# Optimization experiments

Hardware: AMD Instinct MI355X
Metric: run time of the kernel (lower is better)

The kernel has to match this reference:

```python
import jax, jax.numpy as jnp
import numpy as np

N_EMBD = 1024
N_HEADS = 16
HEAD_SIZE = N_EMBD // N_HEADS
BLOCK_SIZE = 2048
BATCH = 2
SEQ = 2048
EPS = 1e-5


def setup_inputs() -> dict:
    key = jax.random.key(0)
    ks = jax.random.split(key, 12)
    s = 0.02
    x = jax.random.normal(ks[0], (BATCH, SEQ, N_EMBD), dtype=jnp.float32)
    # per-head Q/K/V weights concatenated: [n_embd, n_heads*head_size]
    Wq = jax.random.normal(ks[1], (N_EMBD, N_EMBD), dtype=jnp.float32) * s
    Wk = jax.random.normal(ks[2], (N_EMBD, N_EMBD), dtype=jnp.float32) * s
    Wv = jax.random.normal(ks[3], (N_EMBD, N_EMBD), dtype=jnp.float32) * s
    Wproj = jax.random.normal(ks[4], (N_EMBD, N_EMBD), dtype=jnp.float32) * s
    bproj = jnp.zeros((N_EMBD,), dtype=jnp.float32)
    W1 = jax.random.normal(ks[5], (N_EMBD, 4 * N_EMBD), dtype=jnp.float32) * s
    b1 = jnp.zeros((4 * N_EMBD,), dtype=jnp.float32)
    W2 = jax.random.normal(ks[6], (4 * N_EMBD, N_EMBD), dtype=jnp.float32) * s
    b2 = jnp.zeros((N_EMBD,), dtype=jnp.float32)
    ln1_w = jnp.ones((N_EMBD,), dtype=jnp.float32)
    ln1_b = jnp.zeros((N_EMBD,), dtype=jnp.float32)
    ln2_w = jnp.ones((N_EMBD,), dtype=jnp.float32)
    ln2_b = jnp.zeros((N_EMBD,), dtype=jnp.float32)
    return dict(x=x, Wq=Wq, Wk=Wk, Wv=Wv, Wproj=Wproj, bproj=bproj,
                W1=W1, b1=b1, W2=W2, b2=b2,
                ln1_w=ln1_w, ln1_b=ln1_b, ln2_w=ln2_w, ln2_b=ln2_b)


def _layer_norm(x, w, b):
    mu = jnp.mean(x, axis=-1, keepdims=True)
    var = jnp.var(x, axis=-1, keepdims=True)
    return (x - mu) * jax.lax.rsqrt(var + EPS) * w + b


def reference(x, Wq, Wk, Wv, Wproj, bproj, W1, b1, W2, b2, ln1_w, ln1_b, ln2_w, ln2_b):
    B, T, C = x.shape
    # --- attention sub-block (pre-LN) ---
    h = _layer_norm(x, ln1_w, ln1_b)
    # project then split heads: [B,T,H,D] -> [B,H,T,D]
    def split(W):
        return (h @ W).reshape(B, T, N_HEADS, HEAD_SIZE).transpose(0, 2, 1, 3)
    q, k, v = split(Wq), split(Wk), split(Wv)
    # NOTE: original code scales by C**-0.5 with C = n_embd (not head_size)
    scores = jnp.einsum('bhtd,bhsd->bhts', q, k) * (C ** -0.5)  # [B,H,T,T]
    causal = jnp.tril(jnp.ones((T, T), dtype=bool))
    scores = jnp.where(causal, scores, -jnp.inf)
    wei = jax.nn.softmax(scores, axis=-1)
    attn = jnp.einsum('bhts,bhsd->bhtd', wei, v)  # [B,H,T,D]
    attn = attn.transpose(0, 2, 1, 3).reshape(B, T, C)  # concat heads
    x = x + attn @ Wproj + bproj
    # --- FFN sub-block (pre-LN) ---
    h2 = _layer_norm(x, ln2_w, ln2_b)
    ff = jax.nn.relu(h2 @ W1 + b1) @ W2 + b2
    return x + ff
```

## Files before the change

### kernel.cpp

```cpp
#include <hip/hip_runtime.h>
#include <cstdint>

typedef __attribute__((ext_vector_type(8))) __bf16 bf16_8;
typedef __attribute__((ext_vector_type(4))) __bf16 bf16_4;
typedef __attribute__((ext_vector_type(4))) float f32x4;

#define QSCALE 0.045084220027780106f

__device__ __forceinline__ void gld_lds16(const __bf16* g, __bf16* l) {
  __builtin_amdgcn_global_load_lds(
      (const __attribute__((address_space(1))) void*)(void*)g,
      (__attribute__((address_space(3))) void*)l, 16, 0, 0);
}

__global__ __launch_bounds__(256) void convt_k(
    const float* __restrict__ Wq, const float* __restrict__ Wk,
    const float* __restrict__ Wv, const float* __restrict__ Wp,
    const float* __restrict__ W1, const float* __restrict__ W2,
    __bf16* __restrict__ WqT, __bf16* __restrict__ WkT,
    __bf16* __restrict__ WvT, __bf16* __restrict__ WpT,
    __bf16* __restrict__ W1T, __bf16* __restrict__ W2T) {
  int bid = blockIdx.x;
  const float* in; __bf16* outp; int Kd, Nd, tile;
  if (bid < 4096) {
    int m = bid >> 10; tile = bid & 1023; Kd = 1024; Nd = 1024;
    in   = m == 0 ? Wq  : m == 1 ? Wk  : m == 2 ? Wv  : Wp;
    outp = m == 0 ? WqT : m == 1 ? WkT : m == 2 ? WvT : WpT;
  } else if (bid < 8192) {
    tile = bid - 4096; Kd = 1024; Nd = 4096; in = W1; outp = W1T;
  } else {
    tile = bid - 8192; Kd = 4096; Nd = 1024; in = W2; outp = W2T;
  }
  int tilesN = Nd >> 5;
  int tk = tile / tilesN, tn = tile % tilesN;
  int k0 = tk * 32, n0 = tn * 32;
  __shared__ float tbuf[32][33];
  int tx = threadIdx.x & 31, ty = threadIdx.x >> 5;
#pragma unroll
  for (int i = 0; i < 4; ++i)
    tbuf[ty + i * 8][tx] = in[(size_t)(k0 + ty + i * 8) * Nd + (n0 + tx)];
  __syncthreads();
#pragma unroll
  for (int i = 0; i < 4; ++i)
    outp[(size_t)(n0 + ty + i * 8) * Kd + (k0 + tx)] = (__bf16)tbuf[tx][ty + i * 8];
}

__global__ __launch_bounds__(256) void ln_k(const float* __restrict__ x,
                                            const float* __restrict__ w,
                                            const float* __restrict__ b,
                                            __bf16* __restrict__ out) {
  int row = blockIdx.x;
  int tid = threadIdx.x;
  f32x4 v = *(const f32x4*)(x + (size_t)row * 1024 + tid * 4);
  float s = v[0] + v[1] + v[2] + v[3];
  float sq = v[0] * v[0] + v[1] * v[1] + v[2] * v[2] + v[3] * v[3];
#pragma unroll
  for (int m = 1; m < 64; m <<= 1) { s += __shfl_xor(s, m); sq += __shfl_xor(sq, m); }
  __shared__ float rs[4], rq[4];
  int wave = tid >> 6, lane = tid & 63;
  if (lane == 0) { rs[wave] = s; rq[wave] = sq; }
  __syncthreads();
  s  = rs[0] + rs[1] + rs[2] + rs[3];
  sq = rq[0] + rq[1] + rq[2] + rq[3];
  float mu   = s * (1.f / 1024.f);
  float var  = sq * (1.f / 1024.f) - mu * mu;
  float rstd = rsqrtf(var + 1e-5f);
  f32x4 wv = *(const f32x4*)(w + tid * 4);
  f32x4 bv = *(const f32x4*)(b + tid * 4);
  bf16_4 o;
#pragma unroll
  for (int i = 0; i < 4; ++i) o[i] = (__bf16)((v[i] - mu) * rstd * wv[i] + bv[i]);
  *(bf16_4*)(out + (size_t)row * 1024 + tid * 4) = o;
}

template <int MODE, int BM, int BN, int BK>
__global__ __launch_bounds__(256) void gemm_k(
    const __bf16* __restrict__ A,
    const __bf16* __restrict__ B0, const __bf16* __restrict__ B1,
    const __bf16* __restrict__ B2,
    __bf16* __restrict__ O0, __bf16* __restrict__ O1, __bf16* __restrict__ O2,
    float* __restrict__ Of,
    const float* __restrict__ bias, const float* __restrict__ res,
    int K, int Nchunk, int nBlkM, int nBlkN) {
  constexpr int NC = BK / 8;
  constexpr int MT = BM / 32, NT = BN / 32;
  constexpr int KK = BK / 32;
  constexpr int RPC = 64 / NC;
  constexpr int CA = BM / RPC / 4;
  constexpr int CB = BN / RPC / 4;
  __shared__ __align__(16) __bf16 As[2][BM * BK];
  __shared__ __align__(16) __bf16 Bs[2][BN * BK];
  int chunk = blockIdx.y;
  const __bf16* Bt = chunk == 0 ? B0 : (chunk == 1 ? B1 : B2);
  __bf16* Ob       = chunk == 0 ? O0 : (chunk == 1 ? O1 : O2);
  int pid = blockIdx.x;
  const int GM = 8;
  int perG = GM * nBlkN;
  int gid = pid / perG;
  int fm = gid * GM;
  int gsz = min(nBlkM - fm, GM);
  int bm = fm + (pid % gsz);
  int bn = (pid % perG) / gsz;
  int m0 = bm * BM, n0 = bn * BN;
  int tid = threadIdx.x, wave = tid >> 6, lane = tid & 63;
  int quad = lane >> 4, l16 = lane & 15;
  int wm = (wave & 1) * (BM / 2), wn = (wave >> 1) * (BN / 2);
  int srow = lane / NC, schunk = lane % NC;

  f32x4 z = {0.f, 0.f, 0.f, 0.f};
  f32x4 acc[MT][NT];
#pragma unroll
  for (int mt = 0; mt < MT; ++mt)
#pragma unroll
    for (int nt = 0; nt < NT; ++nt) acc[mt][nt] = z;

  const __bf16* Ag = A  + (size_t)m0 * K;
  const __bf16* Bg = Bt + (size_t)n0 * K;

  auto stage = [&](int k0, int buf) {
#pragma unroll
    for (int i = 0; i < CA; ++i) {
      int r0 = (wave * CA + i) * RPC;
      int gc = schunk ^ ((r0 + srow) & (NC - 1));
      gld_lds16(Ag + (size_t)(r0 + srow) * K + k0 + gc * 8, &As[buf][r0 * BK]);
    }
#pragma unroll
    for (int i = 0; i < CB; ++i) {
      int r0 = (wave * CB + i) * RPC;
      int gc = schunk ^ ((r0 + srow) & (NC - 1));
      gld_lds16(Bg + (size_t)(r0 + srow) * K + k0 + gc * 8, &Bs[buf][r0 * BK]);
    }
  };

  auto compute = [&](int buf) {
#pragma unroll
    for (int kk = 0; kk < KK; ++kk) {
      bf16_8 af[MT], bfr[NT];
#pragma unroll
      for (int t = 0; t < MT; ++t) {
        int r = wm + t * 16 + l16;
        int lc = (kk * 4 + quad) ^ (r & (NC - 1));
        af[t] = *(const bf16_8*)(&As[buf][r * BK + lc * 8]);
      }
#pragma unroll
      for (int t = 0; t < NT; ++t) {
        int r = wn + t * 16 + l16;
        int lc = (kk * 4 + quad) ^ (r & (NC - 1));
        bfr[t] = *(const bf16_8*)(&Bs[buf][r * BK + lc * 8]);
      }
#pragma unroll
      for (int mt = 0; mt < MT; ++mt)
#pragma unroll
        for (int nt = 0; nt < NT; ++nt)
          acc[mt][nt] = __builtin_amdgcn_mfma_f32_16x16x32_bf16(af[mt], bfr[nt],
                                                                acc[mt][nt], 0, 0, 0);
    }
  };

  int niter = K / BK;
  stage(0, 0);
  __syncthreads();
  for (int it = 0; it < niter - 1; ++it) {
    stage((it + 1) * BK, (it + 1) & 1);
    compute(it & 1);
    __syncthreads();
  }
  compute((niter - 1) & 1);

  if (MODE == 0 && chunk == 2) {
#pragma unroll
    for (int mt = 0; mt < MT; ++mt) {
      int mbase = m0 + wm + mt * 16 + quad * 4;
      int bb = mbase >> 11, tt = mbase & 2047;
#pragma unroll
      for (int nt = 0; nt < NT; ++nt) {
        int n = n0 + wn + nt * 16 + l16;
        bf16_4 pk;
#pragma unroll
        for (int r = 0; r < 4; ++r) pk[r] = (__bf16)acc[mt][nt][r];
        *(bf16_4*)(O2 + ((size_t)((bb * 16 + (n >> 6)) * 64 + (n & 63))) * 2048 + tt) = pk;
      }
    }
    return;
  }

  float oscale = (MODE == 0 && chunk == 0) ? QSCALE : 1.0f;
#pragma unroll
  for (int mt = 0; mt < MT; ++mt) {
#pragma unroll
    for (int r = 0; r < 4; ++r) {
      int m = m0 + wm + mt * 16 + quad * 4 + r;
      size_t rowo = (size_t)m * Nchunk;
#pragma unroll
      for (int nt = 0; nt < NT; ++nt) {
        int n = n0 + wn + nt * 16 + l16;
        float v = acc[mt][nt][r];
        if (MODE == 0) {
          Ob[rowo + n] = (__bf16)(v * oscale);
        } else if (MODE == 1) {
          v += bias[n]; v = v > 0.f ? v : 0.f;
          Ob[rowo + n] = (__bf16)v;
        } else {
          v += bias[n] + res[rowo + n];
          Of[rowo + n] = v;
        }
      }
    }
  }
}

__global__ __launch_bounds__(256) void attn_k(const __bf16* __restrict__ Q,
                                              const __bf16* __restrict__ K,
                                              const __bf16* __restrict__ Vt,
                                              __bf16* __restrict__ O) {
  __shared__ __align__(16) __bf16 Pls[4][32 * 72];
  __shared__ __align__(16) float Obuf[2][32][68];
  __shared__ float Lbuf[2][32][4];

  int i = blockIdx.x;
  int bh = i & 31, p = i >> 5;
  int h = bh & 15, b = bh >> 4;
  int tid = threadIdx.x, wave = tid >> 6, lane = tid & 63;
  int quad = lane >> 4, l16 = lane & 15;
  int pr = wave >> 1;
  int roleB = wave & 1;
  int j = pr == 0 ? p : 31 - p;
  int qg_lo = j, qg_hi = 63 - j;
  int t_lo = (j >> 1) + 1;
  int t_hi = 32 - (j >> 1);
  int ksp = 17 - t_lo;

  const __bf16* Kb = K + (size_t)(b * 2048) * 1024 + h * 64;
  const __bf16* Vh = Vt + (size_t)((b * 16 + h) * 64) * 2048;
  __bf16* Pw = &Pls[wave][0];

  f32x4 z = {0.f, 0.f, 0.f, 0.f};
  bf16_8 qf[2][2];
  f32x4 ot[2][4];
  float l_acc[2];

  auto loadQ = [&](int qg) {
#pragma unroll
    for (int g = 0; g < 2; ++g) {
      const __bf16* Qg = Q + ((size_t)(b * 2048 + qg * 32 + g * 16 + l16)) * 1024 + h * 64;
      qf[g][0] = *(const bf16_8*)(Qg + quad * 8);
      qf[g][1] = *(const bf16_8*)(Qg + 32 + quad * 8);
    }
  };

  auto zacc = [&]() {
#pragma unroll
    for (int g = 0; g < 2; ++g) {
#pragma unroll
      for (int dt = 0; dt < 4; ++dt) ot[g][dt] = z;
      l_acc[g] = 0.f;
    }
  };

  auto process = [&](int qg, int it0, int it1) {
    int qw = qg * 32;
    for (int it = it0; it < it1; ++it) {
      int kt = it * 64;
      bool masked = (kt + 63 > qw);
      bf16_8 kfr[4][2], vfr[4][2];
#pragma unroll
      for (int kk = 0; kk < 4; ++kk) {
        const __bf16* kr = Kb + (size_t)(kt + kk * 16 + l16) * 1024 + quad * 8;
        kfr[kk][0] = *(const bf16_8*)(kr);
        kfr[kk][1] = *(const bf16_8*)(kr + 32);
      }
#pragma unroll
      for (int dt = 0; dt < 4; ++dt) {
        const __bf16* vr = Vh + (size_t)(dt * 16 + l16) * 2048 + kt + quad * 8;
        vfr[dt][0] = *(const bf16_8*)(vr);
        vfr[dt][1] = *(const bf16_8*)(vr + 32);
      }
      f32x4 sf[2][4];
#pragma unroll
      for (int kk = 0; kk < 4; ++kk) {
#pragma unroll
        for (int g = 0; g < 2; ++g) {
          f32x4 a = z;
          a = __builtin_amdgcn_mfma_f32_16x16x32_bf16(kfr[kk][0], qf[g][0], a, 0, 0, 0);
          a = __builtin_amdgcn_mfma_f32_16x16x32_bf16(kfr[kk][1], qf[g][1], a, 0, 0, 0);
          sf[g][kk] = a;
        }
      }
#pragma unroll
      for (int g = 0; g < 2; ++g) {
        int qrow = qw + g * 16 + l16;
#pragma unroll
        for (int kk = 0; kk < 4; ++kk) {
          bf16_4 pk;
#pragma unroll
          for (int r = 0; r < 4; ++r) {
            float x = sf[g][kk][r];
            if (masked && (kt + kk * 16 + quad * 4 + r > qrow)) x = -1e30f;
            float pp = __builtin_amdgcn_exp2f(x);
            l_acc[g] += pp;
            pk[r] = (__bf16)pp;
          }
          *(bf16_4*)(Pw + (g * 16 + l16) * 72 + kk * 16 + quad * 4) = pk;
        }
      }
      bf16_8 pf[2][2];
#pragma unroll
      for (int g = 0; g < 2; ++g) {
        pf[g][0] = *(const bf16_8*)(Pw + (g * 16 + l16) * 72 + quad * 8);
        pf[g][1] = *(const bf16_8*)(Pw + (g * 16 + l16) * 72 + 32 + quad * 8);
      }
#pragma unroll
      for (int dt = 0; dt < 4; ++dt) {
#pragma unroll
        for (int g = 0; g < 2; ++g) {
          ot[g][dt] = __builtin_amdgcn_mfma_f32_16x16x32_bf16(vfr[dt][0], pf[g][0], ot[g][dt], 0, 0, 0);
          ot[g][dt] = __builtin_amdgcn_mfma_f32_16x16x32_bf16(vfr[dt][1], pf[g][1], ot[g][dt], 0, 0, 0);
        }
      }
    }
  };

  auto writeO = [&](int qg, const float* lc) {
#pragma unroll
    for (int g = 0; g < 2; ++g) {
      float l = lc[g];
      l += __shfl_xor(l, 16);
      l += __shfl_xor(l, 32);
      float inv = 1.0f / l;
      size_t base = (size_t)(b * 2048 + qg * 32 + g * 16 + l16) * 1024 + h * 64;
#pragma unroll
      for (int dt = 0; dt < 4; ++dt) {
        bf16_4 ok;
#pragma unroll
        for (int r = 0; r < 4; ++r) ok[r] = (__bf16)(ot[g][dt][r] * inv);
        *(bf16_4*)(O + base + dt * 16 + quad * 4) = ok;
      }
    }
  };

  if (roleB) {
    loadQ(qg_hi); zacc();
    process(qg_hi, ksp, t_hi);
#pragma unroll
    for (int g = 0; g < 2; ++g) {
#pragma unroll
      for (int dt = 0; dt < 4; ++dt)
        *(f32x4*)&Obuf[pr][g * 16 + l16][dt * 16 + quad * 4] = ot[g][dt];
      Lbuf[pr][g * 16 + l16][quad] = l_acc[g];
    }
  } else {
    loadQ(qg_lo); zacc();
    process(qg_lo, 0, t_lo);
    writeO(qg_lo, l_acc);
    loadQ(qg_hi); zacc();
    process(qg_hi, 0, ksp);
  }
  __syncthreads();
  if (!roleB) {
#pragma unroll
    for (int g = 0; g < 2; ++g) {
#pragma unroll
      for (int dt = 0; dt < 4; ++dt)
        ot[g][dt] += *(const f32x4*)&Obuf[pr][g * 16 + l16][dt * 16 + quad * 4];
    }
    float lc[2];
#pragma unroll
    for (int g = 0; g < 2; ++g) lc[g] = l_acc[g] + Lbuf[pr][g * 16 + l16][quad];
    writeO(qg_hi, lc);
  }
}

extern "C" void kernel_launch(void* const* d_in, const int* in_sizes, int n_in,
                              void* d_out, int out_size, void* d_ws,
                              size_t ws_size, hipStream_t stream) {
  const float* x   = (const float*)d_in[0];
  const float* Wq  = (const float*)d_in[1];
  const float* Wk  = (const float*)d_in[2];
  const float* Wv  = (const float*)d_in[3];
  const float* Wp  = (const float*)d_in[4];
  const float* bp  = (const float*)d_in[5];
  const float* W1  = (const float*)d_in[6];
  const float* b1  = (const float*)d_in[7];
  const float* W2  = (const float*)d_in[8];
  const float* b2  = (const float*)d_in[9];
  const float* l1w = (const float*)d_in[10];
  const float* l1b = (const float*)d_in[11];
  const float* l2w = (const float*)d_in[12];
  const float* l2b = (const float*)d_in[13];
  float* out = (float*)d_out;
  char* ws = (char*)d_ws;
  const size_t MB = 1024ull * 1024ull;
  __bf16* WqT = (__bf16*)(ws + 0 * MB);
  __bf16* WkT = (__bf16*)(ws + 2 * MB);
  __bf16* WvT = (__bf16*)(ws + 4 * MB);
  __bf16* WpT = (__bf16*)(ws + 6 * MB);
  __bf16* W1T = (__bf16*)(ws + 8 * MB);
  __bf16* W2T = (__bf16*)(ws + 16 * MB);
  __bf16* hb  = (__bf16*)(ws + 24 * MB);
  __bf16* Qb  = (__bf16*)(ws + 32 * MB);
  __bf16* Kb_ = (__bf16*)(ws + 40 * MB);
  __bf16* Vt  = (__bf16*)(ws + 48 * MB);
  __bf16* Ab  = (__bf16*)(ws + 56 * MB);
  __bf16* F1  = (__bf16*)(ws + 64 * MB);

  convt_k<<<12288, 256, 0, stream>>>(Wq, Wk, Wv, Wp, W1, W2,
                                     WqT, WkT, WvT, WpT, W1T, W2T);
  ln_k<<<4096, 256, 0, stream>>>(x, l1w, l1b, hb);
  gemm_k<0, 128, 128, 32><<<dim3(256, 3), 256, 0, stream>>>(
      hb, WqT, WkT, WvT, Qb, Kb_, Vt, nullptr, nullptr, nullptr,
      1024, 1024, 32, 8);
  attn_k<<<512, 256, 0, stream>>>(Qb, Kb_, Vt, Ab);
  gemm_k<2, 64, 64, 64><<<dim3(1024, 1), 256, 0, stream>>>(
      Ab, WpT, WpT, WpT, nullptr, nullptr, nullptr, out, bp, x,
      1024, 1024, 64, 16);
  ln_k<<<4096, 256, 0, stream>>>(out, l2w, l2b, hb);
  gemm_k<1, 128, 128, 32><<<dim3(1024, 1), 256, 0, stream>>>(
      hb, W1T, W1T, W1T, F1, F1, F1, nullptr, b1, nullptr,
      1024, 4096, 32, 32);
  gemm_k<2, 64, 64, 64><<<dim3(1024, 1), 256, 0, stream>>>(
      F1, W2T, W2T, W2T, nullptr, nullptr, nullptr, out, b2, out,
      4096, 1024, 64, 16);
}
```

Measured before the change: 351.6 us.

## Split attention key range across four waves per query pair and prefetch K

The attention kernel now pairs one low and one high query group per block, doubling the grid. The 33 key tiles are split evenly across the four waves, and the partial outputs are combined through LDS in bf16. K fragments for the next tile are prefetched during softmax, and launch bounds request higher occupancy. This is meant to balance causal work across waves and hide global load latency, at the cost of bf16 rounding on the partial sums and more LDS traffic.

Result: slower. 365.1 us (+3.8%).

```diff
diff --git a/kernel.cpp b/kernel.cpp
--- a/kernel.cpp
+++ b/kernel.cpp
@@ -209,72 +209,72 @@
   }
 }
 
-__global__ __launch_bounds__(256) void attn_k(const __bf16* __restrict__ Q,
-                                              const __bf16* __restrict__ K,
-                                              const __bf16* __restrict__ Vt,
-                                              __bf16* __restrict__ O) {
+__global__ __launch_bounds__(256, 4) void attn_k(const __bf16* __restrict__ Q,
+                                                 const __bf16* __restrict__ K,
+                                                 const __bf16* __restrict__ Vt,
+                                                 __bf16* __restrict__ O) {
   __shared__ __align__(16) __bf16 Pls[4][32 * 72];
-  __shared__ __align__(16) float Obuf[2][32][68];
-  __shared__ float Lbuf[2][32][4];
+  __shared__ __align__(16) __bf16 Xbuf[2][32 * 72];
+  __shared__ float Lbuf[4][32][4];
 
   int i = blockIdx.x;
-  int bh = i & 31, p = i >> 5;
+  int bh = i & 31, j = i >> 5;
   int h = bh & 15, b = bh >> 4;
   int tid = threadIdx.x, wave = tid >> 6, lane = tid & 63;
   int quad = lane >> 4, l16 = lane & 15;
-  int pr = wave >> 1;
-  int roleB = wave & 1;
-  int j = pr == 0 ? p : 31 - p;
   int qg_lo = j, qg_hi = 63 - j;
   int t_lo = (j >> 1) + 1;
-  int t_hi = 32 - (j >> 1);
-  int ksp = 17 - t_lo;
+  int u0 = wave == 0 ? 0 : wave == 1 ? 9 : wave == 2 ? 17 : 25;
+  int u1 = wave == 0 ? 9 : wave == 1 ? 17 : wave == 2 ? 25 : 33;
+  int lo0 = u0, lo1 = min(u1, t_lo);
+  int hi0 = max(u0, t_lo) - t_lo, hi1 = u1 - t_lo;
 
   const __bf16* Kb = K + (size_t)(b * 2048) * 1024 + h * 64;
   const __bf16* Vh = Vt + (size_t)((b * 16 + h) * 64) * 2048;
   __bf16* Pw = &Pls[wave][0];
 
   f32x4 z = {0.f, 0.f, 0.f, 0.f};
-  bf16_8 qf[2][2];
+  bf16_8 qf[2][2], kfr[4][2], vfr[4][2];
   f32x4 ot[2][4];
   float l_acc[2];
 
-  auto loadQ = [&](int qg) {
+  auto loadK = [&](int kt) {
+#pragma unroll
+    for (int kk = 0; kk < 4; ++kk) {
+      const __bf16* kr = Kb + (size_t)(kt + kk * 16 + l16) * 1024 + quad * 8;
+      kfr[kk][0] = *(const bf16_8*)(kr);
+      kfr[kk][1] = *(const bf16_8*)(kr + 32);
+    }
+  };
+  auto loadV = [&](int kt) {
+#pragma unroll
+    for (int dt = 0; dt < 4; ++dt) {
+      const __bf16* vr = Vh + (size_t)(dt * 16 + l16) * 2048 + kt + quad * 8;
+      vfr[dt][0] = *(const bf16_8*)(vr);
+      vfr[dt][1] = *(const bf16_8*)(vr + 32);
+    }
+  };
+
+  auto run = [&](int qg, int it0, int it1) {
 #pragma unroll
     for (int g = 0; g < 2; ++g) {
       const __bf16* Qg = Q + ((size_t)(b * 2048 + qg * 32 + g * 16 + l16)) * 1024 + h * 64;
       qf[g][0] = *(const bf16_8*)(Qg + quad * 8);
       qf[g][1] = *(const bf16_8*)(Qg + 32 + quad * 8);
     }
-  };
-
-  auto zacc = [&]() {
 #pragma unroll
     for (int g = 0; g < 2; ++g) {
 #pragma unroll
       for (int dt = 0; dt < 4; ++dt) ot[g][dt] = z;
       l_acc[g] = 0.f;
     }
-  };
-
-  auto process = [&](int qg, int it0, int it1) {
+    if (it0 >= it1) return;
     int qw = qg * 32;
+    loadK(it0 * 64);
     for (int it = it0; it < it1; ++it) {
       int kt = it * 64;
+      loadV(kt);
       bool masked = (kt + 63 > qw);
-      bf16_8 kfr[4][2], vfr[4][2];
-#pragma unroll
-      for (int kk = 0; kk < 4; ++kk) {
-        const __bf16* kr = Kb + (size_t)(kt + kk * 16 + l16) * 1024 + quad * 8;
-        kfr[kk][0] = *(const bf16_8*)(kr);
-        kfr[kk][1] = *(const bf16_8*)(kr + 32);
-      }
-#pragma unroll
-      for (int dt = 0; dt < 4; ++dt) {
-        const __bf16* vr = Vh + (size_t)(dt * 16 + l16) * 2048 + kt + quad * 8;
-        vfr[dt][0] = *(const bf16_8*)(vr);
-        vfr[dt][1] = *(const bf16_8*)(vr + 32);
-      }
       f32x4 sf[2][4];
 #pragma unroll
       for (int kk = 0; kk < 4; ++kk) {
@@ -286,6 +286,7 @@
           sf[g][kk] = a;
         }
       }
+      loadK(it + 1 < it1 ? (it + 1) * 64 : kt);
 #pragma unroll
       for (int g = 0; g < 2; ++g) {
         int qrow = qw + g * 16 + l16;
@@ -320,10 +321,35 @@
     }
   };
 
-  auto writeO = [&](int qg, const float* lc) {
+  auto putP = [&](__bf16* Ob, float (*Lb)[4]) {
 #pragma unroll
     for (int g = 0; g < 2; ++g) {
-      float l = lc[g];
+#pragma unroll
+      for (int dt = 0; dt < 4; ++dt) {
+        bf16_4 pk;
+#pragma unroll
+        for (int r = 0; r < 4; ++r) pk[r] = (__bf16)ot[g][dt][r];
+        *(bf16_4*)(Ob + (g * 16 + l16) * 72 + dt * 16 + quad * 4) = pk;
+      }
+      Lb[g * 16 + l16][quad] = l_acc[g];
+    }
+  };
+  auto addP = [&](const __bf16* Ob, const float (*Lb)[4]) {
+#pragma unroll
+    for (int g = 0; g < 2; ++g) {
+#pragma unroll
+      for (int dt = 0; dt < 4; ++dt) {
+        bf16_4 pk = *(const bf16_4*)(Ob + (g * 16 + l16) * 72 + dt * 16 + quad * 4);
+#pragma unroll
+        for (int r = 0; r < 4; ++r) ot[g][dt][r] += (float)pk[r];
+      }
+      l_acc[g] += Lb[g * 16 + l16][quad];
+    }
+  };
+  auto writeO = [&](int qg) {
+#pragma unroll
+    for (int g = 0; g < 2; ++g) {
+      float l = l_acc[g];
       l += __shfl_xor(l, 16);
       l += __shfl_xor(l, 32);
       float inv = 1.0f / l;
@@ -338,35 +364,30 @@
     }
   };
 
-  if (roleB) {
-    loadQ(qg_hi); zacc();
-    process(qg_hi, ksp, t_hi);
-#pragma unroll
-    for (int g = 0; g < 2; ++g) {
-#pragma unroll
-      for (int dt = 0; dt < 4; ++dt)
-        *(f32x4*)&Obuf[pr][g * 16 + l16][dt * 16 + quad * 4] = ot[g][dt];
-      Lbuf[pr][g * 16 + l16][quad] = l_acc[g];
-    }
+  if (wave == 0) {
+    run(qg_hi, hi0, hi1);
+    putP(&Xbuf[0][0], Lbuf[0]);
+    run(qg_lo, lo0, lo1);
+    __syncthreads();
+    addP(&Xbuf[1][0], Lbuf[1]);
+    writeO(qg_lo);
+  } else if (wave == 1) {
+    run(qg_lo, lo0, lo1);
+    putP(&Xbuf[1][0], Lbuf[1]);
+    run(qg_hi, hi0, hi1);
+    putP(&Pls[1][0], Lbuf[2]);
+    __syncthreads();
+  } else if (wave == 2) {
+    run(qg_hi, hi0, hi1);
+    putP(&Pls[2][0], Lbuf[3]);
+    __syncthreads();
   } else {
-    loadQ(qg_lo); zacc();
-    process(qg_lo, 0, t_lo);
-    writeO(qg_lo, l_acc);
-    loadQ(qg_hi); zacc();
-    process(qg_hi, 0, ksp);
-  }
-  __syncthreads();
-  if (!roleB) {
-#pragma unroll
-    for (int g = 0; g < 2; ++g) {
-#pragma unroll
-      for (int dt = 0; dt < 4; ++dt)
-        ot[g][dt] += *(const f32x4*)&Obuf[pr][g * 16 + l16][dt * 16 + quad * 4];
-    }
-    float lc[2];
-#pragma unroll
-    for (int g = 0; g < 2; ++g) lc[g] = l_acc[g] + Lbuf[pr][g * 16 + l16][quad];
-    writeO(qg_hi, lc);
+    run(qg_hi, hi0, hi1);
+    __syncthreads();
+    addP(&Pls[1][0], Lbuf[2]);
+    addP(&Pls[2][0], Lbuf[3]);
+    addP(&Xbuf[0][0], Lbuf[0]);
+    writeO(qg_hi);
   }
 }
 
@@ -409,7 +430,7 @@
   gemm_k<0, 128, 128, 32><<<dim3(256, 3), 256, 0, stream>>>(
       hb, WqT, WkT, WvT, Qb, Kb_, Vt, nullptr, nullptr, nullptr,
       1024, 1024, 32, 8);
-  attn_k<<<512, 256, 0, stream>>>(Qb, Kb_, Vt, Ab);
+  attn_k<<<1024, 256, 0, stream>>>(Qb, Kb_, Vt, Ab);
   gemm_k<2, 64, 64, 64><<<dim3(1024, 1), 256, 0, stream>>>(
       Ab, WpT, WpT, WpT, nullptr, nullptr, nullptr, out, bp, x,
       1024, 1024, 64, 16);
```
